# Optimization experiments

Measured on AMD Instinct MI355X. Metric: run time of the kernel, lower is better.

## Reference

```python
import jax, jax.numpy as jnp
import numpy as np


def setup_inputs() -> dict:
    key = jax.random.key(0)
    k1, k2, k3 = jax.random.split(key, 3)
    B, N, D = 4, 4096, 256
    val = jax.random.normal(k1, (B, N, D), dtype=jnp.float32)
    state = jax.random.normal(k2, (B, N), dtype=jnp.float32)
    # val projection weight, scaled for unit-variance outputs
    Wv = jax.random.normal(k3, (D, D), dtype=jnp.float32) / np.sqrt(D)
    return {"val": val, "state": state, "Wv": Wv}


def reference(val, state, Wv):
    # pairwise_fn: dot-product scores over all node pairs -> [B, N, N]
    scores = jnp.einsum("bnd,bmd->bnm", val, val)
    # edge_compress_fn: softsign (non-softmax elementwise nonlinearity)
    edges = scores / (1.0 + jnp.abs(scores))
    # state_proj_fn = identity, val_proj_fn = linear
    projected_state = state                                  # [B, N]
    projected_val = jnp.einsum("bmd,de->bme", val, Wv)       # [B, N, D]
    # dual aggregation reusing the same edge matrix
    delta_state = jnp.einsum("bnm,bm->bn", edges, projected_state)
    delta_val = jnp.einsum("bnm,bmd->bnd", edges, projected_val)
    return (delta_state, delta_val)
```

## Files before the change

kernel.cpp:

```cpp
#include <hip/hip_runtime.h>

typedef unsigned short u16;
typedef unsigned char u8;
typedef unsigned int u32;
typedef __bf16 bf16x8 __attribute__((ext_vector_type(8)));
typedef float  f32x16 __attribute__((ext_vector_type(16)));
typedef int    i32x4  __attribute__((ext_vector_type(4)));
typedef int    i32x16 __attribute__((ext_vector_type(16)));

#define NB 4
#define NN 4096
#define ND 256

#define QPV (127.0f / 4.5f)
#define DPV (4.5f / 16129.0f)
#define QST (127.0f / 4.6f)
#define DST (4.6f / 16129.0f)
#define MAGIC 12582912.0f

__device__ __forceinline__ u16 f2bf(float x) { return __builtin_bit_cast(u16, (__bf16)x); }
__device__ __forceinline__ u32 fbits(float x) { return __builtin_bit_cast(u32, x); }

__device__ __forceinline__ u32 packlow4(float a, float b, float c, float d) {
    u32 p = __builtin_amdgcn_perm(fbits(b), fbits(a), 0x00000400u);
    u32 q = __builtin_amdgcn_perm(fbits(d), fbits(c), 0x00000400u);
    return __builtin_amdgcn_perm(q, p, 0x05040100u);
}



__global__ __launch_bounds__(256) void k_wv(const float* __restrict__ Wv, u16* __restrict__ wv) {
    __shared__ u16 t2[256 * 33];
    int tid = threadIdx.x;
    int es = blockIdx.x, e0 = es * 32;
    #pragma unroll
    for (int k = 0; k < 8; k++) {
        int idx = tid + k * 256;
        int row = idx >> 3, c4 = idx & 7;
        float4 v = *(const float4*)(Wv + row * 256 + e0 + c4 * 4);
        u16* p = t2 + row * 33 + c4 * 4;
        p[0] = f2bf(v.x); p[1] = f2bf(v.y); p[2] = f2bf(v.z); p[3] = f2bf(v.w);
    }
    __syncthreads();
    u16* dst = wv + (size_t)es * 16 * 512;
    #pragma unroll
    for (int k = 0; k < 4; k++) {
        int flat = tid + k * 256;
        int s = flat >> 6, l = flat & 63;
        int l31 = l & 31, h = l >> 5;
        union { u16 o[8]; uint4 q; } u;
        #pragma unroll
        for (int j = 0; j < 8; j++) u.o[j] = t2[(s * 16 + h * 8 + j) * 33 + l31];
        *(uint4*)(dst + (size_t)flat * 8) = u.q;
    }
}

__global__ __launch_bounds__(256) void k_prep(const float* __restrict__ val,
                                              const float* __restrict__ state,
                                              const u16* __restrict__ wvf,
                                              u8* __restrict__ kq8,
                                              float* __restrict__ srow,
                                              u8* __restrict__ vp8) {
    int tid = threadIdx.x;
    int bid = blockIdx.x;
    if (bid < 512) {
        __shared__ float t[32 * 257];
        __shared__ float rmax[32];
        const float* src = val + (size_t)bid * 32 * 256;
        #pragma unroll
        for (int k = 0; k < 8; k++) {
            int idx = tid + k * 256;
            int row = idx >> 6, c4 = idx & 63;
            float4 v = *(const float4*)(src + row * 256 + c4 * 4);
            float* p = t + row * 257 + c4 * 4;
            p[0] = v.x; p[1] = v.y; p[2] = v.z; p[3] = v.w;
        }
        __syncthreads();
        {
            int row = tid >> 3, seg = tid & 7;
            float m = 0.0f;
            #pragma unroll
            for (int i = 0; i < 32; i++) m = fmaxf(m, fabsf(t[row * 257 + seg + i * 8]));
            m = fmaxf(m, __shfl_down(m, 4));
            m = fmaxf(m, __shfl_down(m, 2));
            m = fmaxf(m, __shfl_down(m, 1));
            if (seg == 0) {
                m = fmaxf(m, 1e-20f);
                rmax[row] = m;
                srow[bid * 32 + row] = m * (1.0f / 127.0f);
            }
        }
        __syncthreads();
        u8* dst8 = kq8 + (size_t)bid * 8192;
        #pragma unroll
        for (int k = 0; k < 2; k++) {
            int flat = tid + k * 256;
            int s = flat >> 6, l = flat & 63;
            int l31 = l & 31, h = l >> 5;
            float r127 = 127.0f / rmax[l31];
            const float* p = t + l31 * 257 + s * 32 + h * 16;
            u32 d[4];
            #pragma unroll
            for (int g = 0; g < 4; g++)
                d[g] = packlow4(fmaf(p[4 * g + 0], r127, MAGIC), fmaf(p[4 * g + 1], r127, MAGIC),
                                fmaf(p[4 * g + 2], r127, MAGIC), fmaf(p[4 * g + 3], r127, MAGIC));
            *(uint4*)(dst8 + (size_t)flat * 16) = make_uint4(d[0], d[1], d[2], d[3]);
        }
        {
            int w = tid >> 6, lane = tid & 63;
            int l31 = lane & 31, h = lane >> 5;
            const u16* wv0 = wvf + ((size_t)((w * 2 + 0) * 16)) * 512 + lane * 8;
            const u16* wv1 = wvf + ((size_t)((w * 2 + 1) * 16)) * 512 + lane * 8;
            f32x16 acc0 = {}, acc1 = {};
            for (int s = 0; s < 16; s++) {
                union { u16 o[8]; bf16x8 v; } ua;
                const float* p = t + l31 * 257 + s * 16 + h * 8;
                #pragma unroll
                for (int j = 0; j < 8; j++) ua.o[j] = f2bf(p[j]);
                bf16x8 b0 = *(const bf16x8*)(wv0 + (size_t)s * 512);
                bf16x8 b1 = *(const bf16x8*)(wv1 + (size_t)s * 512);
                acc0 = __builtin_amdgcn_mfma_f32_32x32x16_bf16(ua.v, b0, acc0, 0, 0, 0);
                acc1 = __builtin_amdgcn_mfma_f32_32x32x16_bf16(ua.v, b1, acc1, 0, 0, 0);
            }
            union { u32 wd[4]; i32x4 v; } o0, o1;
            #pragma unroll
            for (int g = 0; g < 4; g++) {
                o0.wd[g] = packlow4(
                    fminf(fmaxf(acc0[4 * g + 0] * QPV, -127.0f), 127.0f) + MAGIC,
                    fminf(fmaxf(acc0[4 * g + 1] * QPV, -127.0f), 127.0f) + MAGIC,
                    fminf(fmaxf(acc0[4 * g + 2] * QPV, -127.0f), 127.0f) + MAGIC,
                    fminf(fmaxf(acc0[4 * g + 3] * QPV, -127.0f), 127.0f) + MAGIC);
                o1.wd[g] = packlow4(
                    fminf(fmaxf(acc1[4 * g + 0] * QPV, -127.0f), 127.0f) + MAGIC,
                    fminf(fmaxf(acc1[4 * g + 1] * QPV, -127.0f), 127.0f) + MAGIC,
                    fminf(fmaxf(acc1[4 * g + 2] * QPV, -127.0f), 127.0f) + MAGIC,
                    fminf(fmaxf(acc1[4 * g + 3] * QPV, -127.0f), 127.0f) + MAGIC);
            }
            *(i32x4*)(vp8 + ((size_t)(bid * 9 + w * 2 + 0)) * 1024 + lane * 16) = o0.v;
            *(i32x4*)(vp8 + ((size_t)(bid * 9 + w * 2 + 1)) * 1024 + lane * 16) = o1.v;
        }
    } else {
        int b = bid - 512;
        __shared__ u8 qs[4096];
        #pragma unroll
        for (int k = 0; k < 16; k++) {
            int i = tid + k * 256;
            float x = fminf(fmaxf(state[b * 4096 + i] * QST, -127.0f), 127.0f);
            qs[i] = (u8)(fbits(x + MAGIC) & 255);
        }
        __syncthreads();
        #pragma unroll
        for (int k = 0; k < 32; k++) {
            int chunk = tid + k * 256;
            int strip = chunk >> 6, lane = chunk & 63, h = (lane >> 5) & 1;
            union { u32 wd[4]; i32x4 v; } u;
            #pragma unroll
            for (int g = 0; g < 4; g++)
                u.wd[g] = *(const u32*)(qs + strip * 32 + 8 * g + 4 * h);
            *(i32x4*)(vp8 + ((size_t)((b * 128 + strip) * 9 + 8)) * 1024 + (chunk & 63) * 16) = u.v;
        }
    }
}

__global__ __launch_bounds__(256, 2) void k_main(const u8* __restrict__ kq8,
                                                 const u8* __restrict__ vp8,
                                                 const float* __restrict__ srow,
                                                 float* __restrict__ ds_out,
                                                 float* __restrict__ dval_out) {
    __shared__ i32x4 pbuf[2][4][64];
    __shared__ int dsqi[4][32];

    int tid = threadIdx.x;
    int w = tid >> 6, lane = tid & 63;
    int l31 = lane & 31, h = lane >> 5;

    int id = blockIdx.x;
    int xcd = id & 7;
    int bb = xcd >> 1;
    int t7 = ((xcd & 1) << 6) | (id >> 3);
    int q0 = t7 * 32;
    size_t bbase = (size_t)bb * 128;

    i32x4 qf[8];
    {
        const u8* qsrc = kq8 + (bbase + t7) * 8192 + lane * 16;
        #pragma unroll
        for (int s = 0; s < 8; s++) qf[s] = *(const i32x4*)(qsrc + (size_t)s * 1024);
    }
    float srq = srow[bb * 4096 + q0 + l31];

    i32x16 oacc[2] = {};
    i32x16 dsa = {};

    i32x4 kf[8], vf[4][2], sf;
    float4 sg[4];
    {
        const u8* kb = kq8 + (bbase + w) * 8192 + lane * 16;
        #pragma unroll
        for (int s = 0; s < 8; s++) kf[s] = *(const i32x4*)(kb + (size_t)s * 1024);
        #pragma unroll
        for (int st = 0; st < 4; st++)
            #pragma unroll
            for (int e = 0; e < 2; e++)
                vf[st][e] = *(const i32x4*)(vp8 + ((size_t)((bbase + st) * 9 + 2 * w + e)) * 1024 + lane * 16);
        sf = *(const i32x4*)(vp8 + ((size_t)((bbase + w) * 9 + 8)) * 1024 + lane * 16);
        const float* srm = srow + bb * 4096 + w * 32;
        #pragma unroll
        for (int g = 0; g < 4; g++) sg[g] = *(const float4*)(srm + g * 8 + h * 4);
    }

    for (int mt = 0; mt < 32; mt++) {
        i32x16 s0 = {}, s1 = {};
        #pragma unroll
        for (int s = 0; s < 8; s += 2) {
            s0 = __builtin_amdgcn_mfma_i32_32x32x32_i8(kf[s], qf[s], s0, 0, 0, 0);
            s1 = __builtin_amdgcn_mfma_i32_32x32x32_i8(kf[s + 1], qf[s + 1], s1, 0, 0, 0);
        }
        if (mt + 1 < 32) {
            const u8* kb = kq8 + (bbase + (mt + 1) * 4 + w) * 8192 + lane * 16;
            #pragma unroll
            for (int s = 0; s < 8; s++) kf[s] = *(const i32x4*)(kb + (size_t)s * 1024);
        }

        float cf[16];
        #pragma unroll
        for (int r = 0; r < 16; r++) {
            float sm = ((const float*)&sg[r >> 2])[r & 3] * srq;
            float xs = (float)(s0[r] + s1[r]) * sm;
            float p = xs * __builtin_amdgcn_rcpf(1.0f + fabsf(xs));
            cf[r] = fmaf(p, 127.0f, MAGIC);
        }
        if (mt + 1 < 32) {
            const float* srm = srow + bb * 4096 + (mt + 1) * 128 + w * 32;
            #pragma unroll
            for (int g = 0; g < 4; g++) sg[g] = *(const float4*)(srm + g * 8 + h * 4);
        }
        union { u32 wd[4]; i32x4 v; } pu;
        pu.wd[0] = packlow4(cf[0], cf[1], cf[2], cf[3]);
        pu.wd[1] = packlow4(cf[4], cf[5], cf[6], cf[7]);
        pu.wd[2] = packlow4(cf[8], cf[9], cf[10], cf[11]);
        pu.wd[3] = packlow4(cf[12], cf[13], cf[14], cf[15]);
        i32x4 pf = pu.v;

        dsa = __builtin_amdgcn_mfma_i32_32x32x32_i8(pf, sf, dsa, 0, 0, 0);
        if (mt + 1 < 32)
            sf = *(const i32x4*)(vp8 + ((size_t)((bbase + (mt + 1) * 4 + w) * 9 + 8)) * 1024 + lane * 16);

        pbuf[mt & 1][w][lane] = pf;
        __syncthreads();
        i32x4 pl[4];
        #pragma unroll
        for (int st = 0; st < 4; st++) pl[st] = pbuf[mt & 1][st][lane];

        #pragma unroll
        for (int st = 0; st < 4; st++) {
            oacc[0] = __builtin_amdgcn_mfma_i32_32x32x32_i8(pl[st], vf[st][0], oacc[0], 0, 0, 0);
            oacc[1] = __builtin_amdgcn_mfma_i32_32x32x32_i8(pl[st], vf[st][1], oacc[1], 0, 0, 0);
        }
        if (mt + 1 < 32) {
            #pragma unroll
            for (int st = 0; st < 4; st++)
                #pragma unroll
                for (int e = 0; e < 2; e++)
                    vf[st][e] = *(const i32x4*)(vp8 + ((size_t)((bbase + (mt + 1) * 4 + st) * 9 + 2 * w + e)) * 1024 + lane * 16);
        }
    }

    if (l31 == 0) {
        #pragma unroll
        for (int r = 0; r < 16; r++) dsqi[w][(r & 3) + 8 * (r >> 2) + 4 * h] = dsa[r];
    }
    #pragma unroll
    for (int e = 0; e < 2; e++) {
        #pragma unroll
        for (int r = 0; r < 16; r++) {
            int row = (r & 3) + 8 * (r >> 2) + 4 * h;
            dval_out[((size_t)(bb * 4096 + q0 + row)) * 256 + (2 * w + e) * 32 + l31] =
                (float)oacc[e][r] * DPV;
        }
    }
    __syncthreads();
    if (w == 0 && lane < 32) {
        int d = dsqi[0][lane] + dsqi[1][lane] + dsqi[2][lane] + dsqi[3][lane];
        ds_out[bb * 4096 + q0 + lane] = (float)d * DST;
    }
}

extern "C" void kernel_launch(void* const* d_in, const int* in_sizes, int n_in,
                              void* d_out, int out_size, void* d_ws, size_t ws_size,
                              hipStream_t stream) {
    const float* val   = (const float*)d_in[0];
    const float* state = (const float*)d_in[1];
    const float* Wv    = (const float*)d_in[2];

    float* ds_out   = (float*)d_out;
    float* dval_out = ds_out + NB * NN;

    u8*  kq8 = (u8*)d_ws;
    u8*  vp8 = kq8 + (size_t)NB * NN * ND;
    u16* wv  = (u16*)(vp8 + (size_t)NB * 128 * 9216);
    float* srow = (float*)(wv + 8 * 16 * 512);

    k_wv<<<8, 256, 0, stream>>>(Wv, wv);
    k_prep<<<516, 256, 0, stream>>>(val, state, wv, kq8, srow, vp8);
    k_main<<<512, 256, 0, stream>>>(kq8, vp8, srow, ds_out, dval_out);
}
```

Before: 135.0 us.

## Split waves into score producers and PV consumers with double-buffered LDS handoff

Turns the uniform four-wave loop into a warp-specialized pipeline. Two waves compute QK scores, softsign, int8 packing and the state aggregation for two key strips each, and write them into a double-buffered LDS tile one step ahead. The other two waves consume the previous tile and run the P·V MFMAs over four output column groups each. The aim is to overlap the score and elementwise stage with the value-aggregation MFMAs. The cost is that producer K loads are no longer prefetched, each producer wave now runs two strips serially, and the consumers carry more accumulators and V fragments, raising register pressure.

```diff
diff --git a/kernel.cpp b/kernel.cpp
--- a/kernel.cpp
+++ b/kernel.cpp
@@ -168,7 +168,7 @@
                                                  float* __restrict__ ds_out,
                                                  float* __restrict__ dval_out) {
     __shared__ i32x4 pbuf[2][4][64];
-    __shared__ int dsqi[4][32];
+    __shared__ int dsqi[2][32];
 
     int tid = threadIdx.x;
     int w = tid >> 6, lane = tid & 63;
@@ -181,108 +181,111 @@
     int q0 = t7 * 32;
     size_t bbase = (size_t)bb * 128;
 
-    i32x4 qf[8];
-    {
-        const u8* qsrc = kq8 + (bbase + t7) * 8192 + lane * 16;
-        #pragma unroll
-        for (int s = 0; s < 8; s++) qf[s] = *(const i32x4*)(qsrc + (size_t)s * 1024);
-    }
-    float srq = srow[bb * 4096 + q0 + l31];
-
-    i32x16 oacc[2] = {};
-    i32x16 dsa = {};
-
-    i32x4 kf[8], vf[4][2], sf;
-    float4 sg[4];
-    {
-        const u8* kb = kq8 + (bbase + w) * 8192 + lane * 16;
-        #pragma unroll
-        for (int s = 0; s < 8; s++) kf[s] = *(const i32x4*)(kb + (size_t)s * 1024);
+    if (w < 2) {
+        int p = w;
+        i32x4 qf[8];
+        {
+            const u8* qsrc = kq8 + (bbase + t7) * 8192 + lane * 16;
+            #pragma unroll
+            for (int s = 0; s < 8; s++) qf[s] = *(const i32x4*)(qsrc + (size_t)s * 1024);
+        }
+        float srq = srow[bb * 4096 + q0 + l31];
+        i32x16 dsa = {};
+
+        auto produce = [&](int tt) {
+            #pragma unroll
+            for (int half = 0; half < 2; half++) {
+                int strip = tt * 4 + 2 * p + half;
+                const u8* kb = kq8 + (bbase + strip) * 8192 + lane * 16;
+                i32x4 kf[8];
+                #pragma unroll
+                for (int s = 0; s < 8; s++) kf[s] = *(const i32x4*)(kb + (size_t)s * 1024);
+                const float* srm = srow + bb * 4096 + strip * 32;
+                float4 sg[4];
+                #pragma unroll
+                for (int g = 0; g < 4; g++) sg[g] = *(const float4*)(srm + g * 8 + h * 4);
+                i32x4 sf = *(const i32x4*)(vp8 + ((size_t)((bbase + strip) * 9 + 8)) * 1024 + lane * 16);
+
+                i32x16 s0 = {}, s1 = {};
+                #pragma unroll
+                for (int s = 0; s < 8; s += 2) {
+                    s0 = __builtin_amdgcn_mfma_i32_32x32x32_i8(kf[s], qf[s], s0, 0, 0, 0);
+                    s1 = __builtin_amdgcn_mfma_i32_32x32x32_i8(kf[s + 1], qf[s + 1], s1, 0, 0, 0);
+                }
+                float cf[16];
+                #pragma unroll
+                for (int r = 0; r < 16; r++) {
+                    float sm = ((const float*)&sg[r >> 2])[r & 3] * srq;
+                    float xs = (float)(s0[r] + s1[r]) * sm;
+                    float pp = xs * __builtin_amdgcn_rcpf(1.0f + fabsf(xs));
+                    cf[r] = fmaf(pp, 127.0f, MAGIC);
+                }
+                union { u32 wd[4]; i32x4 v; } pu;
+                pu.wd[0] = packlow4(cf[0], cf[1], cf[2], cf[3]);
+                pu.wd[1] = packlow4(cf[4], cf[5], cf[6], cf[7]);
+                pu.wd[2] = packlow4(cf[8], cf[9], cf[10], cf[11]);
+                pu.wd[3] = packlow4(cf[12], cf[13], cf[14], cf[15]);
+                dsa = __builtin_amdgcn_mfma_i32_32x32x32_i8(pu.v, sf, dsa, 0, 0, 0);
+                pbuf[tt & 1][2 * p + half][lane] = pu.v;
+            }
+        };
+
+        produce(0);
+        __syncthreads();
+        for (int mt = 0; mt < 32; mt++) {
+            if (mt + 1 < 32) produce(mt + 1);
+            __syncthreads();
+        }
+        if (l31 == 0) {
+            #pragma unroll
+            for (int r = 0; r < 16; r++) dsqi[p][(r & 3) + 8 * (r >> 2) + 4 * h] = dsa[r];
+        }
+        __syncthreads();
+        if (w == 0 && lane < 32) {
+            int d = dsqi[0][lane] + dsqi[1][lane];
+            ds_out[bb * 4096 + q0 + lane] = (float)d * DST;
+        }
+    } else {
+        int c = w - 2;
+        i32x16 oacc[4] = {};
+        i32x4 vf[4][4];
         #pragma unroll
         for (int st = 0; st < 4; st++)
             #pragma unroll
-            for (int e = 0; e < 2; e++)
-                vf[st][e] = *(const i32x4*)(vp8 + ((size_t)((bbase + st) * 9 + 2 * w + e)) * 1024 + lane * 16);
-        sf = *(const i32x4*)(vp8 + ((size_t)((bbase + w) * 9 + 8)) * 1024 + lane * 16);
-        const float* srm = srow + bb * 4096 + w * 32;
-        #pragma unroll
-        for (int g = 0; g < 4; g++) sg[g] = *(const float4*)(srm + g * 8 + h * 4);
-    }
-
-    for (int mt = 0; mt < 32; mt++) {
-        i32x16 s0 = {}, s1 = {};
-        #pragma unroll
-        for (int s = 0; s < 8; s += 2) {
-            s0 = __builtin_amdgcn_mfma_i32_32x32x32_i8(kf[s], qf[s], s0, 0, 0, 0);
-            s1 = __builtin_amdgcn_mfma_i32_32x32x32_i8(kf[s + 1], qf[s + 1], s1, 0, 0, 0);
-        }
-        if (mt + 1 < 32) {
-            const u8* kb = kq8 + (bbase + (mt + 1) * 4 + w) * 8192 + lane * 16;
-            #pragma unroll
-            for (int s = 0; s < 8; s++) kf[s] = *(const i32x4*)(kb + (size_t)s * 1024);
-        }
-
-        float cf[16];
-        #pragma unroll
-        for (int r = 0; r < 16; r++) {
-            float sm = ((const float*)&sg[r >> 2])[r & 3] * srq;
-            float xs = (float)(s0[r] + s1[r]) * sm;
-            float p = xs * __builtin_amdgcn_rcpf(1.0f + fabsf(xs));
-            cf[r] = fmaf(p, 127.0f, MAGIC);
-        }
-        if (mt + 1 < 32) {
-            const float* srm = srow + bb * 4096 + (mt + 1) * 128 + w * 32;
-            #pragma unroll
-            for (int g = 0; g < 4; g++) sg[g] = *(const float4*)(srm + g * 8 + h * 4);
-        }
-        union { u32 wd[4]; i32x4 v; } pu;
-        pu.wd[0] = packlow4(cf[0], cf[1], cf[2], cf[3]);
-        pu.wd[1] = packlow4(cf[4], cf[5], cf[6], cf[7]);
-        pu.wd[2] = packlow4(cf[8], cf[9], cf[10], cf[11]);
-        pu.wd[3] = packlow4(cf[12], cf[13], cf[14], cf[15]);
-        i32x4 pf = pu.v;
-
-        dsa = __builtin_amdgcn_mfma_i32_32x32x32_i8(pf, sf, dsa, 0, 0, 0);
-        if (mt + 1 < 32)
-            sf = *(const i32x4*)(vp8 + ((size_t)((bbase + (mt + 1) * 4 + w) * 9 + 8)) * 1024 + lane * 16);
-
-        pbuf[mt & 1][w][lane] = pf;
-        __syncthreads();
-        i32x4 pl[4];
-        #pragma unroll
-        for (int st = 0; st < 4; st++) pl[st] = pbuf[mt & 1][st][lane];
-
-        #pragma unroll
-        for (int st = 0; st < 4; st++) {
-            oacc[0] = __builtin_amdgcn_mfma_i32_32x32x32_i8(pl[st], vf[st][0], oacc[0], 0, 0, 0);
-            oacc[1] = __builtin_amdgcn_mfma_i32_32x32x32_i8(pl[st], vf[st][1], oacc[1], 0, 0, 0);
-        }
-        if (mt + 1 < 32) {
-            #pragma unroll
-            for (int st = 0; st < 4; st++)
-                #pragma unroll
-                for (int e = 0; e < 2; e++)
-                    vf[st][e] = *(const i32x4*)(vp8 + ((size_t)((bbase + (mt + 1) * 4 + st) * 9 + 2 * w + e)) * 1024 + lane * 16);
-        }
-    }
-
-    if (l31 == 0) {
-        #pragma unroll
-        for (int r = 0; r < 16; r++) dsqi[w][(r & 3) + 8 * (r >> 2) + 4 * h] = dsa[r];
-    }
-    #pragma unroll
-    for (int e = 0; e < 2; e++) {
-        #pragma unroll
-        for (int r = 0; r < 16; r++) {
-            int row = (r & 3) + 8 * (r >> 2) + 4 * h;
-            dval_out[((size_t)(bb * 4096 + q0 + row)) * 256 + (2 * w + e) * 32 + l31] =
-                (float)oacc[e][r] * DPV;
-        }
-    }
-    __syncthreads();
-    if (w == 0 && lane < 32) {
-        int d = dsqi[0][lane] + dsqi[1][lane] + dsqi[2][lane] + dsqi[3][lane];
-        ds_out[bb * 4096 + q0 + lane] = (float)d * DST;
+            for (int e = 0; e < 4; e++)
+                vf[st][e] = *(const i32x4*)(vp8 + ((size_t)((bbase + st) * 9 + c * 4 + e)) * 1024 + lane * 16);
+
+        __syncthreads();
+        for (int mt = 0; mt < 32; mt++) {
+            i32x4 pl[4];
+            #pragma unroll
+            for (int st = 0; st < 4; st++) pl[st] = pbuf[mt & 1][st][lane];
+
+            #pragma unroll
+            for (int st = 0; st < 4; st++) {
+                #pragma unroll
+                for (int e = 0; e < 4; e++)
+                    oacc[e] = __builtin_amdgcn_mfma_i32_32x32x32_i8(pl[st], vf[st][e], oacc[e], 0, 0, 0);
+            }
+            if (mt + 1 < 32) {
+                #pragma unroll
+                for (int st = 0; st < 4; st++)
+                    #pragma unroll
+                    for (int e = 0; e < 4; e++)
+                        vf[st][e] = *(const i32x4*)(vp8 + ((size_t)((bbase + (mt + 1) * 4 + st) * 9 + c * 4 + e)) * 1024 + lane * 16);
+            }
+            __syncthreads();
+        }
+        #pragma unroll
+        for (int e = 0; e < 4; e++) {
+            #pragma unroll
+            for (int r = 0; r < 16; r++) {
+                int row = (r & 3) + 8 * (r >> 2) + 4 * h;
+                dval_out[((size_t)(bb * 4096 + q0 + row)) * 256 + (c * 4 + e) * 32 + l31] =
+                    (float)oacc[e][r] * DPV;
+            }
+        }
+        __syncthreads();
     }
 }
 
```

Result: slower. 157.8 us (+17.0%).
